# Optimization experiments

Measured on AMD Instinct MI355X. Metric: run time of the kernel, lower is better.

The kernel has to match this reference:

```python
import jax, jax.numpy as jnp
import numpy as np

H = 4                      # num_heads hard-coded in SDHGNN
NAMES = ["self", "cross", "self", "cross"]
POOL_SIZES = [2, 2, 2, 2]
MIN_NGHS = 128             # minium_nghs
EPS = 1e-3                 # InstanceNorm1d eps


def _pw(x, W, b):
    # pointwise Conv1d(kernel=1): [B, Cin, N] -> [B, Cout, N]
    return jnp.einsum('oi,bin->bon', W, x) + b[None, :, None]


def _instnorm(x):
    # InstanceNorm1d (no affine): normalize over N per (B, C)
    m = jnp.mean(x, axis=2, keepdims=True)
    v = jnp.mean((x - m) ** 2, axis=2, keepdims=True)
    return (x - m) * jax.lax.rsqrt(v + EPS)


def _attn_prop(x, src, p):
    # SharedAttentionalPropagation (sharing_attention=False):
    # MultiHeadedAttention + concat + MLP residual update.
    Wq, bq, Wk, bk, Wv, bv, Wm, bm, W1, b1, W2, b2 = p
    B, D, N = x.shape
    dh = D // H
    q = _pw(x, Wq, bq).reshape(B, dh, H, N)
    k = _pw(src, Wk, bk).reshape(B, dh, H, -1)
    v = _pw(src, Wv, bv).reshape(B, dh, H, -1)
    scores = jnp.einsum('bdhn,bdhm->bhnm', q, k) * (dh ** -0.5)
    prob = jax.nn.softmax(scores, axis=-1)                     # [B,H,N,M]
    msg = jnp.einsum('bhnm,bdhm->bdhn', prob, v).reshape(B, D, N)
    msg = _pw(msg, Wm, bm)
    y = jnp.concatenate([x, msg], axis=1)                      # [B,2D,N]
    h = jax.nn.relu(_instnorm(_pw(y, W1, b1)))
    return x + _pw(h, W2, b2), prob


def _gather(x, idx):
    # x: [B,D,N], idx: [B,K] -> [B,D,K]
    return jnp.take_along_axis(
        x, jnp.broadcast_to(idx[:, None, :], (x.shape[0], x.shape[1], idx.shape[1])), axis=2)


def _pool(prob, idx, pool_size):
    # pooling_by_prob (4-D prob branch): mean over heads, sum over queries,
    # top-k by importance, sorted indices, gather global indexes.
    K = idx.shape[1]
    p = prob.mean(axis=1).sum(axis=1)                          # [B,K]
    k = min(max(K // pool_size, MIN_NGHS), K)
    _, top = jax.lax.top_k(p, k)
    top = jnp.sort(top, axis=1)
    return jnp.take_along_axis(idx, top, axis=1)


def setup_inputs() -> dict:
    key = jax.random.key(0)
    B, D, N, L = 2, 128, 2048, 4
    ks = jax.random.split(key, 16)
    s = lambda fan: 1.0 / np.sqrt(fan)
    inp = {
        'x0': jax.random.normal(ks[0], (B, D, N), jnp.float32),
        'x1': jax.random.normal(ks[1], (B, D, N), jnp.float32),
        'Wq': jax.random.normal(ks[2], (L, D, D), jnp.float32) * s(D),
        'bq': jax.random.normal(ks[3], (L, D), jnp.float32) * 0.01,
        'Wk': jax.random.normal(ks[4], (L, D, D), jnp.float32) * s(D),
        'bk': jax.random.normal(ks[5], (L, D), jnp.float32) * 0.01,
        'Wv': jax.random.normal(ks[6], (L, D, D), jnp.float32) * s(D),
        'bv': jax.random.normal(ks[7], (L, D), jnp.float32) * 0.01,
        'Wm': jax.random.normal(ks[8], (L, D, D), jnp.float32) * s(D),
        'bm': jax.random.normal(ks[9], (L, D), jnp.float32) * 0.01,
        'W1': jax.random.normal(ks[10], (L, 2 * D, 2 * D), jnp.float32) * s(2 * D),
        'b1': jax.random.normal(ks[11], (L, 2 * D), jnp.float32) * 0.01,
        'W2': jax.random.normal(ks[12], (L, D, 2 * D), jnp.float32) * s(2 * D),
        'b2': jnp.zeros((L, D), jnp.float32),  # nn.init.constant_(mlp[-1].bias, 0)
    }
    return inp


def reference(x0, x1, Wq, bq, Wk, bk, Wv, bv, Wm, bm, W1, b1, W2, b2):
    B, D, N = x0.shape
    idx0 = jnp.broadcast_to(jnp.arange(N, dtype=jnp.int32)[None], (B, N))
    idx1 = idx0
    for l, (name, ps) in enumerate(zip(NAMES, POOL_SIZES)):
        p = (Wq[l], bq[l], Wk[l], bk[l], Wv[l], bv[l],
             Wm[l], bm[l], W1[l], b1[l], W2[l], b2[l])
        if name == 'self':
            s0, s1 = _gather(x0, idx0), _gather(x1, idx1)
        else:
            s0, s1 = _gather(x1, idx1), _gather(x0, idx0)
        x0, prob0 = _attn_prop(x0, s0, p)
        x1, prob1 = _attn_prop(x1, s1, p)
        if name == 'self':
            idx0 = _pool(prob0, idx0, ps)
            idx1 = _pool(prob1, idx1, ps)
        else:
            idx1 = _pool(prob0, idx1, ps)
            idx0 = _pool(prob1, idx0, ps)
    return jnp.stack([x0, x1], axis=0)   # [2, B, D, N]
```

## Files before the change

kernel.cpp:

```cpp
#include <hip/hip_runtime.h>
#include <cstdint>
#include <cstddef>


#define NB 2
#define ND 128
#define NH 4
#define NN 2048
#define ND2 256
#define DN (ND*NN)
#define BDN (NB*DN)
#define QK_SCALE 0.2550348623f
#define IN_EPS 1e-3f

typedef unsigned short u16;
typedef __attribute__((ext_vector_type(8))) short short8;
typedef __attribute__((ext_vector_type(4))) float f32x4;

__device__ __forceinline__ u16 f2bf(float f) {
    unsigned u = __float_as_uint(f);
    return (u16)((u + 0x7fffu + ((u >> 16) & 1u)) >> 16);
}
__device__ __forceinline__ float bf2f(u16 h) {
    return __uint_as_float(((unsigned)h) << 16);
}
__device__ __forceinline__ float fexp2(float x) {
#if __has_builtin(__builtin_amdgcn_exp2f)
    return __builtin_amdgcn_exp2f(x);
#else
    return exp2f(x);
#endif
}
__device__ __forceinline__ unsigned cvtpk_bf16(float a, float b) {
    unsigned r;
    asm("v_cvt_pk_bf16_f32 %0, %1, %2" : "=v"(r) : "v"(a), "v"(b));
    return r;
}

__global__ __launch_bounds__(256) void init_kernel(
    const float* __restrict__ x0in, const float* __restrict__ x1in,
    float* __restrict__ out, int* __restrict__ idx0, int* __restrict__ idx1)
{
    int tid = blockIdx.x * 256 + threadIdx.x;
    const float4* a = (const float4*)x0in;
    const float4* b = (const float4*)x1in;
    float4* o = (float4*)out;
    o[tid] = a[tid];
    o[BDN/4 + tid] = b[tid];
    if (tid < NB*NN) {
        int v = tid & (NN-1);
        idx0[tid] = v;
        idx1[tid] = v;
    }
}

__global__ __launch_bounds__(256) void wrepack2_kernel(
    const float* __restrict__ Wq, const float* __restrict__ Wk,
    const float* __restrict__ Wv, const float* __restrict__ Wm,
    const float* __restrict__ W1, const float* __restrict__ W2,
    const float* __restrict__ bq, const float* __restrict__ bk,
    const float* __restrict__ bv,
    u16* __restrict__ whi, u16* __restrict__ wlo,
    float* __restrict__ bqp, float* __restrict__ bkp, float* __restrict__ bvp)
{
    int e = blockIdx.x * 256 + threadIdx.x;
    if (e < 655360) {
        int l = e / 163840, r = e - l*163840;
        float v;
        if (r < 49152) {
            int m = r >> 14;
            int rr = r & 16383;
            int o = rr >> 7, c = rr & 127;
            int so = (o & 31)*4 + (o >> 5);
            const float* W = (m == 0) ? Wq : ((m == 1) ? Wk : Wv);
            v = W[l*16384 + so*128 + c];
        } else if (r < 65536) {
            int rr = r - 49152;
            int o = rr >> 7, c = rr & 127;
            int sc = (c & 31)*4 + (c >> 5);
            v = Wm[l*16384 + o*128 + sc];
        } else if (r < 131072) v = W1[l*65536 + r - 65536];
        else                   v = W2[l*32768 + r - 131072];
        u16 hb = f2bf(v);
        whi[e] = hb;
        wlo[e] = f2bf(v - bf2f(hb));
    } else if (e < 656896) {
        int eb = e - 655360;
        int l = eb / 384, rr = eb % 384;
        int which = rr >> 7, o = rr & 127;
        int so = (o & 31)*4 + (o >> 5);
        float v = (which == 0 ? bq : (which == 1 ? bk : bv))[l*128 + so];
        (which == 0 ? bqp : (which == 1 ? bkp : bvp))[l*128 + o] = v;
    }
}

__global__ __launch_bounds__(256) void repack_xh_kernel(
    const float* __restrict__ in, u16* __restrict__ ohi, u16* __restrict__ olo)
{
    __shared__ float tile[32][68];
    int z = blockIdx.y >> 2, cg = blockIdx.y & 3;
    int n0 = blockIdx.x * 64;
    int t = threadIdx.x;
    {
        int i = t >> 3, nc = (t & 7) * 8;
        const float* src = &in[((size_t)z*128 + cg*32 + i)*NN + n0 + nc];
        float4 a = *(const float4*)src;
        float4 b = *(const float4*)(src + 4);
        tile[i][nc+0]=a.x; tile[i][nc+1]=a.y; tile[i][nc+2]=a.z; tile[i][nc+3]=a.w;
        tile[i][nc+4]=b.x; tile[i][nc+5]=b.y; tile[i][nc+6]=b.z; tile[i][nc+7]=b.w;
    }
    __syncthreads();
    int n = t >> 2, c8 = (t & 3) * 8;
    short8 hi, lo;
    #pragma unroll
    for (int j = 0; j < 8; ++j) {
        float v = tile[c8 + j][n];
        u16 h = f2bf(v);
        hi[j] = (short)h;
        lo[j] = (short)f2bf(v - bf2f(h));
    }
    size_t ob = ((size_t)z*NN + n0 + n)*128 + cg*32 + c8;
    *(short8*)&ohi[ob] = hi;
    *(short8*)&olo[ob] = lo;
}

__device__ __forceinline__ void gcore(
    u16* As0, u16* As1, u16* Bs0, u16* Bs1,
    const u16* __restrict__ Whi, const u16* __restrict__ Wlo, int o0, int Cin,
    const u16* __restrict__ B1hi, const u16* __restrict__ B1lo, int s1,
    const u16* __restrict__ B2hi, const u16* __restrict__ B2lo, int s2, int split,
    size_t brow, int n0, const int* __restrict__ idxp, int t, f32x4 acc[2][2])
{
    const int lane = t & 63, w = t >> 6;
    const int l15 = lane & 15, quad = lane >> 4;
    const int wr = (w & 1)*32, wc = (w >> 1)*32;
    const int ao = t >> 2, ak = (t & 3)*8;
    int grow = n0 + ao;
    if (idxp) grow = idxp[grow];

    short8 rA0, rA1, rB0, rB1;
    {
        size_t wa = (size_t)(o0 + ao)*Cin + ak;
        rA0 = *(const short8*)&Whi[wa];
        rA1 = *(const short8*)&Wlo[wa];
        int c = ak;
        const u16 *ph, *pl; size_t off;
        if (c < split) { ph = B1hi; pl = B1lo; off = (brow + grow)*s1 + c; }
        else { ph = B2hi; pl = B2lo; off = (brow + grow)*s2 + (c - split); }
        rB0 = *(const short8*)&ph[off];
        rB1 = *(const short8*)&pl[off];
    }
    for (int kc = 0; kc < Cin; kc += 32) {
        __syncthreads();
        *(short8*)&As0[ao*40 + ak] = rA0;
        *(short8*)&As1[ao*40 + ak] = rA1;
        *(short8*)&Bs0[ao*40 + ak] = rB0;
        *(short8*)&Bs1[ao*40 + ak] = rB1;
        if (kc + 32 < Cin) {
            size_t wa = (size_t)(o0 + ao)*Cin + kc + 32 + ak;
            rA0 = *(const short8*)&Whi[wa];
            rA1 = *(const short8*)&Wlo[wa];
            int c = kc + 32 + ak;
            const u16 *ph, *pl; size_t off;
            if (c < split) { ph = B1hi; pl = B1lo; off = (brow + grow)*s1 + c; }
            else { ph = B2hi; pl = B2lo; off = (brow + grow)*s2 + (c - split); }
            rB0 = *(const short8*)&ph[off];
            rB1 = *(const short8*)&pl[off];
        }
        __syncthreads();
        short8 Ah[2], Al[2], Bh[2], Bl[2];
        #pragma unroll
        for (int a = 0; a < 2; ++a) {
            Ah[a] = *(const short8*)&As0[(wr + a*16 + l15)*40 + quad*8];
            Al[a] = *(const short8*)&As1[(wr + a*16 + l15)*40 + quad*8];
        }
        #pragma unroll
        for (int c = 0; c < 2; ++c) {
            Bh[c] = *(const short8*)&Bs0[(wc + c*16 + l15)*40 + quad*8];
            Bl[c] = *(const short8*)&Bs1[(wc + c*16 + l15)*40 + quad*8];
        }
        #pragma unroll
        for (int a = 0; a < 2; ++a)
            #pragma unroll
            for (int c = 0; c < 2; ++c) {
                acc[a][c] = __builtin_amdgcn_mfma_f32_16x16x32_bf16(Ah[a], Bl[c], acc[a][c], 0,0,0);
                acc[a][c] = __builtin_amdgcn_mfma_f32_16x16x32_bf16(Al[a], Bh[c], acc[a][c], 0,0,0);
                acc[a][c] = __builtin_amdgcn_mfma_f32_16x16x32_bf16(Ah[a], Bh[c], acc[a][c], 0,0,0);
            }
    }
    __syncthreads();
}

__global__ __launch_bounds__(256) void qkv_kernel(
    const u16* __restrict__ Whi, const u16* __restrict__ Wlo,
    const float* __restrict__ bqp, const float* __restrict__ bkp,
    const float* __restrict__ bvp,
    const u16* __restrict__ xphi, const u16* __restrict__ xplo,
    const int* __restrict__ idx0, const int* __restrict__ idx1,
    int cross, int M,
    u16* __restrict__ qthi, u16* __restrict__ qtlo,
    u16* __restrict__ kthi, u16* __restrict__ ktlo,
    u16* __restrict__ vthi, float* __restrict__ p)
{
    __shared__ u16 gsm[10240];
    u16* As0 = gsm;  u16* As1 = gsm + 2560;
    u16* Bs0 = gsm + 5120; u16* Bs1 = gsm + 7680;
    float* tb = (float*)gsm;

    const int z = blockIdx.z;
    const int bx = blockIdx.x;
    const int t = threadIdx.x;
    const int lane = t & 63, w = t >> 6;
    const int l15 = lane & 15, quad = lane >> 4;
    const int wr = (w & 1)*32, wc = (w >> 1)*32;

    int role, o0, n0, nCols;
    const u16 *Wbh, *Wbl;
    const float* bias;
    if (bx < 64) {
        role = 0; o0 = (bx & 1)*64; n0 = (bx >> 1)*64; nCols = NN;
        Wbh = Whi; Wbl = Wlo; bias = bqp;
        if (t < 32) p[(size_t)z*NN + bx*32 + t] = 0.f;
    } else {
        int e = bx - 64;
        int kt = M >> 6;
        int ct = e % kt, rt = e / kt;
        n0 = ct*64; nCols = M;
        if (rt < 2) { role = 1; o0 = rt*64; Wbh = Whi+16384; Wbl = Wlo+16384; bias = bkp; }
        else        { role = 2; o0 = (rt-2)*64; Wbh = Whi+32768; Wbl = Wlo+32768; bias = bvp; }
    }
    size_t brow = (size_t)z * NN;
    const int* idxp = nullptr;
    if (role != 0) {
        int ss = cross ? 1 - (z >> 1) : (z >> 1);
        brow = (size_t)(ss*2 + (z & 1)) * NN;
        idxp = (ss ? idx1 : idx0) + (z & 1)*NN;
    }

    f32x4 acc[2][2];
    #pragma unroll
    for (int a = 0; a < 2; ++a)
        #pragma unroll
        for (int c = 0; c < 2; ++c) acc[a][c] = (f32x4){0.f,0.f,0.f,0.f};

    gcore(As0, As1, Bs0, Bs1, Wbh, Wbl, o0, 128,
          xphi, xplo, 128, xphi, xplo, 128, 128, brow, n0, idxp, t, acc);

    if (role == 2) {
        #pragma unroll
        for (int a = 0; a < 2; ++a)
            #pragma unroll
            for (int c = 0; c < 2; ++c)
                #pragma unroll
                for (int r = 0; r < 4; ++r) {
                    int row = o0 + wr + a*16 + quad*4 + r;
                    int m = n0 + wc + c*16 + l15;
                    float v = acc[a][c][r] + bias[row];
                    vthi[((size_t)(z*4 + (row>>5))*32 + (row&31))*(size_t)M + m] = f2bf(v);
                }
    } else {
        float scale = role ? 1.f : QK_SCALE;
        #pragma unroll
        for (int a = 0; a < 2; ++a)
            #pragma unroll
            for (int c = 0; c < 2; ++c)
                #pragma unroll
                for (int r = 0; r < 4; ++r) {
                    int rl = wr + a*16 + quad*4 + r;
                    tb[rl*66 + wc + c*16 + l15] = acc[a][c][r] + bias[o0 + rl];
                }
        __syncthreads();
        u16* ohi = role ? kthi : qthi;
        u16* olo = role ? ktlo : qtlo;
        int n = t >> 2, rb = (t & 3)*16;
        #pragma unroll
        for (int g = 0; g < 2; ++g) {
            short8 hi, lo;
            #pragma unroll
            for (int j = 0; j < 8; ++j) {
                float v = tb[(rb + g*8 + j)*66 + n] * scale;
                u16 hb = f2bf(v);
                hi[j] = (short)hb;
                lo[j] = (short)f2bf(v - bf2f(hb));
            }
            int rowg = o0 + rb + g*8;
            size_t ob = ((size_t)(z*4 + (rowg >> 5))*nCols + n0 + n)*32 + (rowg & 31);
            *(short8*)&ohi[ob] = hi;
            *(short8*)&olo[ob] = lo;
        }
    }
}

__global__ __launch_bounds__(512, 4) void attn4_kernel(
    const u16* __restrict__ qthi, const u16* __restrict__ qtlo,
    const u16* __restrict__ kthi, const u16* __restrict__ ktlo,
    const u16* __restrict__ vthi, int M,
    u16* __restrict__ msghi, u16* __restrict__ msglo, float* __restrict__ p)
{
    __shared__ u16 kv[14592];
    __shared__ float pcol[2048];
    __shared__ float redm[4][64], redl[4][64];
    __shared__ float rowM[64], rowIV[64];

    u16* ks0 = kv;
    u16* ks1 = kv + 5120;
    u16* vs  = kv + 10240;
    float* obuf = (float*)kv;

    const int t = threadIdx.x;
    const int lane = t & 63, wave = t >> 6;
    const int l15 = lane & 15, quad = lane >> 4;
    const int qp = wave & 1, mh = wave >> 1;
    const int h = blockIdx.y, z = blockIdx.z;
    const int zh = z*4 + h;
    const int n0 = blockIdx.x * 64;

    for (int i = t; i < M; i += 512) pcol[i] = 0.f;

    short8 qBh[2], qBl[2];
    #pragma unroll
    for (int qt = 0; qt < 2; ++qt) {
        size_t qb = ((size_t)zh*NN + n0 + qp*32 + qt*16 + l15)*32 + quad*8;
        qBh[qt] = *(const short8*)&qthi[qb];
        qBl[qt] = *(const short8*)&qtlo[qb];
    }

    const int nch = M >> 7;
    const int sr = t >> 2, sc8 = (t & 3)*8;
    const int vr = t >> 4, vc8 = (t & 15)*8;

    float rm[2] = {-1e30f, -1e30f}, rl[2] = {0.f, 0.f};

    short8 skh, skl, sv;
    {
        size_t gk = ((size_t)zh*M + sr)*32 + sc8;
        skh = *(const short8*)&kthi[gk];
        skl = *(const short8*)&ktlo[gk];
    }

    for (int ch = 0; ch < nch; ++ch) {
        __syncthreads();
        *(short8*)&ks0[sr*40 + sc8] = skh;
        *(short8*)&ks1[sr*40 + sc8] = skl;
        if (ch + 1 < nch) {
            size_t gk = ((size_t)zh*M + ((ch+1) << 7) + sr)*32 + sc8;
            skh = *(const short8*)&kthi[gk];
            skl = *(const short8*)&ktlo[gk];
        }
        __syncthreads();
        #pragma unroll
        for (int qt = 0; qt < 2; ++qt)
            #pragma unroll
            for (int mt = 0; mt < 2; ++mt) {
                int mrow = mh*32 + mt*16 + l15;
                short8 kh = *(const short8*)&ks0[mrow*40 + quad*8];
                short8 kl = *(const short8*)&ks1[mrow*40 + quad*8];
                f32x4 a = {0.f,0.f,0.f,0.f};
                a = __builtin_amdgcn_mfma_f32_16x16x32_bf16(kh, qBl[qt], a, 0,0,0);
                a = __builtin_amdgcn_mfma_f32_16x16x32_bf16(kl, qBh[qt], a, 0,0,0);
                a = __builtin_amdgcn_mfma_f32_16x16x32_bf16(kh, qBh[qt], a, 0,0,0);
                float bm = fmaxf(fmaxf(a[0],a[1]), fmaxf(a[2],a[3]));
                float bs = fexp2(a[0]-bm)+fexp2(a[1]-bm)+fexp2(a[2]-bm)+fexp2(a[3]-bm);
                if (bm > rm[qt]) { rl[qt] = rl[qt]*fexp2(rm[qt]-bm) + bs; rm[qt] = bm; }
                else rl[qt] += bs*fexp2(bm - rm[qt]);
            }
    }

    {
        size_t gk = ((size_t)zh*M + sr)*32 + sc8;
        skh = *(const short8*)&kthi[gk];
        skl = *(const short8*)&ktlo[gk];
        sv  = *(const short8*)&vthi[((size_t)zh*32 + vr)*M + vc8];
    }

    #pragma unroll
    for (int qt = 0; qt < 2; ++qt) {
        #pragma unroll
        for (int off = 16; off <= 32; off <<= 1) {
            float om = __shfl_xor(rm[qt], off);
            float ol = __shfl_xor(rl[qt], off);
            float nm = fmaxf(rm[qt], om);
            rl[qt] = rl[qt]*fexp2(rm[qt]-nm) + ol*fexp2(om-nm);
            rm[qt] = nm;
        }
        if (quad == 0) {
            redm[mh][qp*32 + qt*16 + l15] = rm[qt];
            redl[mh][qp*32 + qt*16 + l15] = rl[qt];
        }
    }
    __syncthreads();
    if (t < 64) {
        float m = redm[0][t], l = redl[0][t];
        #pragma unroll
        for (int w2 = 1; w2 < 4; ++w2) {
            float om = redm[w2][t];
            float nm = fmaxf(m, om);
            l = l*fexp2(m - nm) + redl[w2][t]*fexp2(om - nm);
            m = nm;
        }
        rowM[t] = m;
        rowIV[t] = 1.f / l;
    }
    __syncthreads();
    float myRM[2], myRIV[2];
    #pragma unroll
    for (int qt = 0; qt < 2; ++qt) {
        myRM[qt]  = rowM[qp*32 + qt*16 + l15];
        myRIV[qt] = rowIV[qp*32 + qt*16 + l15];
    }

    f32x4 oa[2][2];
    #pragma unroll
    for (int qt = 0; qt < 2; ++qt)
        #pragma unroll
        for (int dt = 0; dt < 2; ++dt) oa[qt][dt] = (f32x4){0.f,0.f,0.f,0.f};

    const int aA = (l15 + 32*(quad & 1))*4;
    const int aB = aA + 64;
    const bool mtsel = (quad >= 2);

    for (int ch = 0; ch < nch; ++ch) {
        const int m0 = ch << 7;
        __syncthreads();
        *(short8*)&ks0[sr*40 + sc8] = skh;
        *(short8*)&ks1[sr*40 + sc8] = skl;
        *(short8*)&vs[vr*136 + vc8] = sv;
        if (ch + 1 < nch) {
            int m1 = (ch+1) << 7;
            size_t gk = ((size_t)zh*M + m1 + sr)*32 + sc8;
            skh = *(const short8*)&kthi[gk];
            skl = *(const short8*)&ktlo[gk];
            sv  = *(const short8*)&vthi[((size_t)zh*32 + vr)*M + m1 + vc8];
        }
        __syncthreads();

        float pr[2][2][4];
        #pragma unroll
        for (int qt = 0; qt < 2; ++qt)
            #pragma unroll
            for (int mt = 0; mt < 2; ++mt) {
                int mrow = mh*32 + mt*16 + l15;
                short8 kh = *(const short8*)&ks0[mrow*40 + quad*8];
                short8 kl = *(const short8*)&ks1[mrow*40 + quad*8];
                f32x4 a = {0.f,0.f,0.f,0.f};
                a = __builtin_amdgcn_mfma_f32_16x16x32_bf16(kh, qBl[qt], a, 0,0,0);
                a = __builtin_amdgcn_mfma_f32_16x16x32_bf16(kl, qBh[qt], a, 0,0,0);
                a = __builtin_amdgcn_mfma_f32_16x16x32_bf16(kh, qBh[qt], a, 0,0,0);
                #pragma unroll
                for (int r = 0; r < 4; ++r)
                    pr[qt][mt][r] = fexp2(a[r] - myRM[qt]);
            }

        #pragma unroll
        for (int mt = 0; mt < 2; ++mt)
            #pragma unroll
            for (int r = 0; r < 4; ++r) {
                float ps = pr[0][mt][r]*myRIV[0] + pr[1][mt][r]*myRIV[1];
                ps += __shfl_xor(ps, 1);
                ps += __shfl_xor(ps, 2);
                ps += __shfl_xor(ps, 4);
                ps += __shfl_xor(ps, 8);
                if (l15 == 0)
                    atomicAdd(&pcol[m0 + mh*32 + mt*16 + quad*4 + r], ps);
            }

        short8 vA[2];
        #pragma unroll
        for (int dt = 0; dt < 2; ++dt)
            vA[dt] = *(const short8*)&vs[(dt*16 + l15)*136 + mh*32 + quad*8];

        #pragma unroll
        for (int qt = 0; qt < 2; ++qt) {
            unsigned pk00 = cvtpk_bf16(pr[qt][0][0], pr[qt][0][1]);
            unsigned pk01 = cvtpk_bf16(pr[qt][0][2], pr[qt][0][3]);
            unsigned pk10 = cvtpk_bf16(pr[qt][1][0], pr[qt][1][1]);
            unsigned pk11 = cvtpk_bf16(pr[qt][1][2], pr[qt][1][3]);
            unsigned a0 = (unsigned)__builtin_amdgcn_ds_bpermute(aA, (int)pk00);
            unsigned a1 = (unsigned)__builtin_amdgcn_ds_bpermute(aA, (int)pk01);
            unsigned a2 = (unsigned)__builtin_amdgcn_ds_bpermute(aA, (int)pk10);
            unsigned a3 = (unsigned)__builtin_amdgcn_ds_bpermute(aA, (int)pk11);
            unsigned b0 = (unsigned)__builtin_amdgcn_ds_bpermute(aB, (int)pk00);
            unsigned b1 = (unsigned)__builtin_amdgcn_ds_bpermute(aB, (int)pk01);
            unsigned b2 = (unsigned)__builtin_amdgcn_ds_bpermute(aB, (int)pk10);
            unsigned b3 = (unsigned)__builtin_amdgcn_ds_bpermute(aB, (int)pk11);
            union { unsigned u[4]; short8 s; } fb;
            fb.u[0] = mtsel ? a2 : a0;
            fb.u[1] = mtsel ? a3 : a1;
            fb.u[2] = mtsel ? b2 : b0;
            fb.u[3] = mtsel ? b3 : b1;
            #pragma unroll
            for (int dt = 0; dt < 2; ++dt)
                oa[qt][dt] = __builtin_amdgcn_mfma_f32_16x16x32_bf16(vA[dt], fb.s, oa[qt][dt], 0,0,0);
        }
    }
    __syncthreads();

    if (mh > 0) {
        #pragma unroll
        for (int qt = 0; qt < 2; ++qt)
            #pragma unroll
            for (int dt = 0; dt < 2; ++dt)
                #pragma unroll
                for (int r = 0; r < 4; ++r) {
                    int q = qp*32 + qt*16 + l15;
                    int d = dt*16 + quad*4 + r;
                    obuf[((mh-1)*32 + d)*66 + q] = oa[qt][dt][r];
                }
    }
    __syncthreads();
    if (mh == 0) {
        #pragma unroll
        for (int qt = 0; qt < 2; ++qt)
            #pragma unroll
            for (int dt = 0; dt < 2; ++dt)
                #pragma unroll
                for (int r = 0; r < 4; ++r) {
                    int q = qp*32 + qt*16 + l15;
                    int d = dt*16 + quad*4 + r;
                    float v = oa[qt][dt][r];
                    #pragma unroll
                    for (int w2 = 0; w2 < 3; ++w2)
                        v += obuf[(w2*32 + d)*66 + q];
                    obuf[d*66 + q] = v * myRIV[qt];
                }
    }
    __syncthreads();
    {
        int tt = t & 255;
        int n = tt >> 2, i8 = (tt & 3)*8;
        short8 o8;
        if (t < 256) {
            #pragma unroll
            for (int j = 0; j < 8; ++j) o8[j] = (short)f2bf(obuf[(i8+j)*66 + n]);
            *(short8*)&msghi[((size_t)z*NN + n0 + n)*128 + h*32 + i8] = o8;
        } else {
            #pragma unroll
            for (int j = 0; j < 8; ++j) {
                float v = obuf[(i8+j)*66 + n];
                u16 hb = f2bf(v);
                o8[j] = (short)f2bf(v - bf2f(hb));
            }
            *(short8*)&msglo[((size_t)z*NN + n0 + n)*128 + h*32 + i8] = o8;
        }
    }
    for (int i = t; i < M; i += 512)
        atomicAdd(&p[(size_t)z*NN + i], pcol[i]*0.25f);
}

__global__ __launch_bounds__(256) void wm_kernel(
    const u16* __restrict__ Wmh, const u16* __restrict__ Wml,
    const float* __restrict__ bm,
    const u16* __restrict__ msghi, const u16* __restrict__ msglo,
    u16* __restrict__ m2hi, u16* __restrict__ m2lo,
    float* __restrict__ gsum, float* __restrict__ gsq)
{
    __shared__ u16 gsm[10240];
    u16* As0 = gsm;  u16* As1 = gsm + 2560;
    u16* Bs0 = gsm + 5120; u16* Bs1 = gsm + 7680;
    float* tb = (float*)gsm;

    const int z = blockIdx.z, o0 = blockIdx.y*64, n0 = blockIdx.x*64;
    const int t = threadIdx.x;
    const int lane = t & 63, w = t >> 6;
    const int l15 = lane & 15, quad = lane >> 4;
    const int wr = (w & 1)*32, wc = (w >> 1)*32;

    if (blockIdx.x == 0 && blockIdx.y == 0) {
        gsum[z*256 + t] = 0.f;
        gsq[z*256 + t] = 0.f;
    }

    f32x4 acc[2][2];
    #pragma unroll
    for (int a = 0; a < 2; ++a)
        #pragma unroll
        for (int c = 0; c < 2; ++c) acc[a][c] = (f32x4){0.f,0.f,0.f,0.f};
    gcore(As0, As1, Bs0, Bs1, Wmh, Wml, o0, 128,
          msghi, msglo, 128, msghi, msglo, 128, 128,
          (size_t)z*NN, n0, nullptr, t, acc);

    #pragma unroll
    for (int a = 0; a < 2; ++a)
        #pragma unroll
        for (int c = 0; c < 2; ++c)
            #pragma unroll
            for (int r = 0; r < 4; ++r) {
                int rl = wr + a*16 + quad*4 + r;
                tb[rl*66 + wc + c*16 + l15] = acc[a][c][r] + bm[o0 + rl];
            }
    __syncthreads();
    int n = t >> 2, rb = (t & 3)*16;
    #pragma unroll
    for (int g = 0; g < 2; ++g) {
        short8 hi, lo;
        #pragma unroll
        for (int j = 0; j < 8; ++j) {
            float v = tb[(rb + g*8 + j)*66 + n];
            u16 hb = f2bf(v);
            hi[j] = (short)hb;
            lo[j] = (short)f2bf(v - bf2f(hb));
        }
        size_t ob = ((size_t)z*NN + n0 + n)*128 + o0 + rb + g*8;
        *(short8*)&m2hi[ob] = hi;
        *(short8*)&m2lo[ob] = lo;
    }
}

__global__ __launch_bounds__(256) void w1_kernel(
    const u16* __restrict__ W1h, const u16* __restrict__ W1l,
    const float* __restrict__ b1,
    const u16* __restrict__ xphi, const u16* __restrict__ xplo,
    const u16* __restrict__ m2hi, const u16* __restrict__ m2lo,
    float* __restrict__ zf, float* __restrict__ gsum, float* __restrict__ gsq)
{
    __shared__ u16 gsm[10240];
    u16* As0 = gsm;  u16* As1 = gsm + 2560;
    u16* Bs0 = gsm + 5120; u16* Bs1 = gsm + 7680;

    const int z = blockIdx.z, o0 = blockIdx.y*64, n0 = blockIdx.x*64;
    const int t = threadIdx.x;
    const int lane = t & 63, w = t >> 6;
    const int l15 = lane & 15, quad = lane >> 4;
    const int wr = (w & 1)*32, wc = (w >> 1)*32;

    f32x4 acc[2][2];
    #pragma unroll
    for (int a = 0; a < 2; ++a)
        #pragma unroll
        for (int c = 0; c < 2; ++c) acc[a][c] = (f32x4){0.f,0.f,0.f,0.f};
    gcore(As0, As1, Bs0, Bs1, W1h, W1l, o0, 256,
          xphi, xplo, 128, m2hi, m2lo, 128, 128,
          (size_t)z*NN, n0, nullptr, t, acc);

    float ssum[2][4], ssq[2][4];
    #pragma unroll
    for (int a = 0; a < 2; ++a)
        #pragma unroll
        for (int r = 0; r < 4; ++r) { ssum[a][r] = 0.f; ssq[a][r] = 0.f; }
    #pragma unroll
    for (int a = 0; a < 2; ++a)
        #pragma unroll
        for (int c = 0; c < 2; ++c)
            #pragma unroll
            for (int r = 0; r < 4; ++r) {
                int row = o0 + wr + a*16 + quad*4 + r;
                int n = n0 + wc + c*16 + l15;
                float v = acc[a][c][r] + b1[row];
                zf[((size_t)z*256 + row)*NN + n] = v;
                ssum[a][r] += v;
                ssq[a][r] = fmaf(v, v, ssq[a][r]);
            }
    #pragma unroll
    for (int a = 0; a < 2; ++a)
        #pragma unroll
        for (int r = 0; r < 4; ++r) {
            float s = ssum[a][r], q2 = ssq[a][r];
            #pragma unroll
            for (int o = 1; o < 16; o <<= 1) {
                s  += __shfl_xor(s, o);
                q2 += __shfl_xor(q2, o);
            }
            if (l15 == 0) {
                int row = o0 + wr + a*16 + quad*4 + r;
                atomicAdd(&gsum[z*256 + row], s);
                atomicAdd(&gsq[z*256 + row], q2);
            }
        }
}

__global__ __launch_bounds__(256) void hrepack_kernel(
    const float* __restrict__ zf, const float* __restrict__ gsum,
    const float* __restrict__ gsq, u16* __restrict__ hhi, u16* __restrict__ hlo)
{
    __shared__ float tile[32][68];
    int z = blockIdx.y >> 3, cg = blockIdx.y & 7;
    int n0 = blockIdx.x * 64;
    int t = threadIdx.x;
    {
        int i = t >> 3, nc = (t & 7) * 8;
        int c = cg*32 + i;
        float mean = gsum[z*256 + c] * (1.f/NN);
        float var = gsq[z*256 + c] * (1.f/NN) - mean*mean;
        float iv = rsqrtf(var + IN_EPS);
        const float* src = &zf[((size_t)z*256 + c)*NN + n0 + nc];
        float4 a = *(const float4*)src;
        float4 b = *(const float4*)(src + 4);
        float vv[8] = {a.x,a.y,a.z,a.w,b.x,b.y,b.z,b.w};
        #pragma unroll
        for (int j = 0; j < 8; ++j) {
            float v = (vv[j] - mean) * iv;
            tile[i][nc + j] = v > 0.f ? v : 0.f;
        }
    }
    __syncthreads();
    int n = t >> 2, c8 = (t & 3) * 8;
    short8 hi, lo;
    #pragma unroll
    for (int j = 0; j < 8; ++j) {
        float v = tile[c8 + j][n];
        u16 hb = f2bf(v);
        hi[j] = (short)hb;
        lo[j] = (short)f2bf(v - bf2f(hb));
    }
    size_t ob = ((size_t)z*NN + n0 + n)*256 + cg*32 + c8;
    *(short8*)&hhi[ob] = hi;
    *(short8*)&hlo[ob] = lo;
}

__global__ __launch_bounds__(256) void w2_kernel(
    const u16* __restrict__ W2h, const u16* __restrict__ W2l,
    const float* __restrict__ b2,
    const u16* __restrict__ hhi, const u16* __restrict__ hlo,
    float* __restrict__ out, u16* __restrict__ xphi, u16* __restrict__ xplo,
    int writeplanes)
{
    __shared__ u16 gsm[10240];
    u16* As0 = gsm;  u16* As1 = gsm + 2560;
    u16* Bs0 = gsm + 5120; u16* Bs1 = gsm + 7680;
    float* tb = (float*)gsm;

    const int z = blockIdx.z, o0 = blockIdx.y*64, n0 = blockIdx.x*64;
    const int t = threadIdx.x;
    const int lane = t & 63, w = t >> 6;
    const int l15 = lane & 15, quad = lane >> 4;
    const int wr = (w & 1)*32, wc = (w >> 1)*32;

    f32x4 acc[2][2];
    #pragma unroll
    for (int a = 0; a < 2; ++a)
        #pragma unroll
        for (int c = 0; c < 2; ++c) acc[a][c] = (f32x4){0.f,0.f,0.f,0.f};
    gcore(As0, As1, Bs0, Bs1, W2h, W2l, o0, 256,
          hhi, hlo, 256, hhi, hlo, 256, 256,
          (size_t)z*NN, n0, nullptr, t, acc);

    #pragma unroll
    for (int a = 0; a < 2; ++a)
        #pragma unroll
        for (int c = 0; c < 2; ++c)
            #pragma unroll
            for (int r = 0; r < 4; ++r) {
                int rl = wr + a*16 + quad*4 + r;
                int rowg = o0 + rl;
                int n = n0 + wc + c*16 + l15;
                size_t oi = ((size_t)z*128 + rowg)*NN + n;
                float v = acc[a][c][r] + b2[rowg] + out[oi];
                out[oi] = v;
                tb[rl*66 + wc + c*16 + l15] = v;
            }
    __syncthreads();
    if (writeplanes) {
        int n = t >> 2, rb = (t & 3)*16;
        #pragma unroll
        for (int g = 0; g < 2; ++g) {
            short8 hi, lo;
            #pragma unroll
            for (int j = 0; j < 8; ++j) {
                float v = tb[(rb + g*8 + j)*66 + n];
                u16 hb = f2bf(v);
                hi[j] = (short)hb;
                lo[j] = (short)f2bf(v - bf2f(hb));
            }
            size_t ob = ((size_t)z*NN + n0 + n)*128 + o0 + rb + g*8;
            *(short8*)&xphi[ob] = hi;
            *(short8*)&xplo[ob] = lo;
        }
    }
}

__global__ __launch_bounds__(256) void rank_kernel(
    const float* __restrict__ p, int* __restrict__ rank, int M)
{
    int zz = blockIdx.y;
    __shared__ float pv[2048];
    for (int i = threadIdx.x; i < M; i += 256) pv[i] = p[(size_t)zz*NN + i];
    __syncthreads();
    int i = blockIdx.x * 256 + threadIdx.x;
    if (i < M) {
        float pi = pv[i];
        int r = 0;
        for (int j = 0; j < M; ++j) {
            float pj = pv[j];
            r += (pj > pi) ? 1 : ((pj == pi && j < i) ? 1 : 0);
        }
        rank[zz*NN + i] = r;
    }
}

__global__ __launch_bounds__(256) void select_kernel(
    const int* __restrict__ rank, int* __restrict__ idx0, int* __restrict__ idx1,
    int M, int k, int cross)
{
    int z = blockIdx.x;
    int st = z >> 1, b = z & 1;
    int ts = cross ? 1 - st : st;
    int* idx = (ts ? idx1 : idx0) + b * NN;
    const int* rk = rank + z * NN;
    __shared__ int sel[2048], idv[2048], sa[2048], sb[2048];
    int t = threadIdx.x;
    for (int i = t; i < M; i += 256) {
        int s = rk[i] < k ? 1 : 0;
        sel[i] = s;
        sa[i] = s;
        idv[i] = idx[i];
    }
    __syncthreads();
    int* src = sa; int* dst = sb;
    for (int off = 1; off < M; off <<= 1) {
        for (int i = t; i < M; i += 256)
            dst[i] = src[i] + (i >= off ? src[i - off] : 0);
        __syncthreads();
        int* tmp = src; src = dst; dst = tmp;
    }
    for (int i = t; i < M; i += 256)
        if (sel[i]) idx[src[i] - 1] = idv[i];
}

extern "C" void kernel_launch(void* const* d_in, const int* in_sizes, int n_in,
                              void* d_out, int out_size, void* d_ws, size_t ws_size,
                              hipStream_t stream)
{
    const float* x0in = (const float*)d_in[0];
    const float* x1in = (const float*)d_in[1];
    const float* Wq = (const float*)d_in[2];
    const float* bq = (const float*)d_in[3];
    const float* Wk = (const float*)d_in[4];
    const float* bk = (const float*)d_in[5];
    const float* Wv = (const float*)d_in[6];
    const float* bv = (const float*)d_in[7];
    const float* Wm = (const float*)d_in[8];
    const float* bm = (const float*)d_in[9];
    const float* W1 = (const float*)d_in[10];
    const float* b1 = (const float*)d_in[11];
    const float* W2 = (const float*)d_in[12];
    const float* b2 = (const float*)d_in[13];

    float* out = (float*)d_out;
    float* ws  = (float*)d_ws;

    const size_t U = 1048576;
    u16* ub   = (u16*)ws;
    u16* xphi = ub;            u16* xplo = ub + U;
    u16* qthi = ub + 2*U;      u16* qtlo = ub + 3*U;
    u16* kthi = ub + 4*U;      u16* ktlo = ub + 5*U;
    u16* vthi = ub + 6*U;
    u16* msghi = ub + 7*U;     u16* msglo = ub + 8*U;
    u16* m2hi = ub + 9*U;      u16* m2lo = ub + 10*U;
    u16* hhi  = ub + 11*U;     u16* hlo = ub + 13*U;
    u16* whi  = ub + 15*U;     u16* wlo = whi + 655360;
    float* zf = (float*)(ub + 2*U);
    float* ft = (float*)(wlo + 655360);
    float* bqp = ft;           float* bkp = ft + 512;      float* bvp = ft + 1024;
    float* gsum = ft + 1536;   float* gsq = ft + 2560;
    float* p = ft + 3584;
    int* idx0 = (int*)(p + 4*NN);
    int* idx1 = idx0 + NB*NN;
    int* rankb = idx1 + NB*NN;

    init_kernel<<<BDN/4/256, 256, 0, stream>>>(x0in, x1in, out, idx0, idx1);
    wrepack2_kernel<<<2566, 256, 0, stream>>>(Wq, Wk, Wv, Wm, W1, W2, bq, bk, bv,
                                              whi, wlo, bqp, bkp, bvp);
    repack_xh_kernel<<<dim3(32, 16), 256, 0, stream>>>(out, xphi, xplo);

    const int Ms[4] = {2048, 1024, 512, 256};
    for (int l = 0; l < 4; ++l) {
        int M = Ms[l];
        int k_new = (M/2 < 128) ? 128 : M/2;
        int cross = l & 1;
        size_t lw = (size_t)l * 163840;
        const u16* Wlh = whi + lw;  const u16* Wll = wlo + lw;

        qkv_kernel<<<dim3(64 + 4*(M/64), 1, 4), 256, 0, stream>>>(
            Wlh, Wll, bqp + l*128, bkp + l*128, bvp + l*128,
            xphi, xplo, idx0, idx1, cross, M,
            qthi, qtlo, kthi, ktlo, vthi, p);

        attn4_kernel<<<dim3(32, NH, 4), 512, 0, stream>>>(
            qthi, qtlo, kthi, ktlo, vthi, M, msghi, msglo, p);

        wm_kernel<<<dim3(32, 2, 4), 256, 0, stream>>>(
            Wlh + 49152, Wll + 49152, bm + l*128,
            msghi, msglo, m2hi, m2lo, gsum, gsq);

        w1_kernel<<<dim3(32, 4, 4), 256, 0, stream>>>(
            Wlh + 65536, Wll + 65536, b1 + l*256,
            xphi, xplo, m2hi, m2lo, zf, gsum, gsq);

        hrepack_kernel<<<dim3(32, 32), 256, 0, stream>>>(zf, gsum, gsq, hhi, hlo);

        w2_kernel<<<dim3(32, 2, 4), 256, 0, stream>>>(
            Wlh + 131072, Wll + 131072, b2 + l*128,
            hhi, hlo, out, xphi, xplo, (l < 3) ? 1 : 0);

        rank_kernel<<<dim3((M+255)/256, 4), 256, 0, stream>>>(p, rankb, M);
        select_kernel<<<4, 256, 0, stream>>>(rankb, idx0, idx1, M, k_new, cross);
    }
}
```

Before: 542.3 us.

## Load K/V fragments directly from global memory in attention kernel, drop LDS staging

The attention kernel no longer stages K and V chunks through shared memory with register prefetch and two barriers per chunk. Each wave instead loads its own MFMA operand fragments straight from global memory (relying on L1/L2 for reuse across waves), and the MFMA groups are wrapped in s_setprio to favor matrix issue. This removes the per-chunk __syncthreads and LDS traffic, at the cost of redundant global loads across waves, less latency hiding without explicit prefetch, and a dedicated obuf array. The final barrier before the obuf write was also removed, which is safe only because obuf no longer aliases the K/V staging buffer.

```diff
diff --git a/kernel.cpp b/kernel.cpp
--- a/kernel.cpp
+++ b/kernel.cpp
@@ -297,15 +297,10 @@
     const u16* __restrict__ vthi, int M,
     u16* __restrict__ msghi, u16* __restrict__ msglo, float* __restrict__ p)
 {
-    __shared__ u16 kv[14592];
     __shared__ float pcol[2048];
+    __shared__ float obuf[96*66];
     __shared__ float redm[4][64], redl[4][64];
     __shared__ float rowM[64], rowIV[64];
-
-    u16* ks0 = kv;
-    u16* ks1 = kv + 5120;
-    u16* vs  = kv + 10240;
-    float* obuf = (float*)kv;
 
     const int t = threadIdx.x;
     const int lane = t & 63, wave = t >> 6;
@@ -326,51 +321,39 @@
     }
 
     const int nch = M >> 7;
-    const int sr = t >> 2, sc8 = (t & 3)*8;
-    const int vr = t >> 4, vc8 = (t & 15)*8;
+    const size_t kb0 = ((size_t)zh*M + mh*32 + l15)*32 + quad*8;
+    const u16* kbh = kthi + kb0;
+    const u16* kbl = ktlo + kb0;
+    const u16* vb = vthi + ((size_t)zh*32 + l15)*M + mh*32 + quad*8;
 
     float rm[2] = {-1e30f, -1e30f}, rl[2] = {0.f, 0.f};
 
-    short8 skh, skl, sv;
-    {
-        size_t gk = ((size_t)zh*M + sr)*32 + sc8;
-        skh = *(const short8*)&kthi[gk];
-        skl = *(const short8*)&ktlo[gk];
-    }
-
     for (int ch = 0; ch < nch; ++ch) {
-        __syncthreads();
-        *(short8*)&ks0[sr*40 + sc8] = skh;
-        *(short8*)&ks1[sr*40 + sc8] = skl;
-        if (ch + 1 < nch) {
-            size_t gk = ((size_t)zh*M + ((ch+1) << 7) + sr)*32 + sc8;
-            skh = *(const short8*)&kthi[gk];
-            skl = *(const short8*)&ktlo[gk];
-        }
-        __syncthreads();
-        #pragma unroll
-        for (int qt = 0; qt < 2; ++qt)
-            #pragma unroll
-            for (int mt = 0; mt < 2; ++mt) {
-                int mrow = mh*32 + mt*16 + l15;
-                short8 kh = *(const short8*)&ks0[mrow*40 + quad*8];
-                short8 kl = *(const short8*)&ks1[mrow*40 + quad*8];
+        const int co = ch*128*32;
+        #pragma unroll
+        for (int mt = 0; mt < 2; ++mt) {
+            short8 kh = *(const short8*)&kbh[co + mt*512];
+            short8 kl = *(const short8*)&kbl[co + mt*512];
+            __builtin_amdgcn_s_setprio(1);
+            f32x4 av[2];
+            #pragma unroll
+            for (int qt = 0; qt < 2; ++qt) {
                 f32x4 a = {0.f,0.f,0.f,0.f};
                 a = __builtin_amdgcn_mfma_f32_16x16x32_bf16(kh, qBl[qt], a, 0,0,0);
                 a = __builtin_amdgcn_mfma_f32_16x16x32_bf16(kl, qBh[qt], a, 0,0,0);
                 a = __builtin_amdgcn_mfma_f32_16x16x32_bf16(kh, qBh[qt], a, 0,0,0);
+                av[qt] = a;
+            }
+            __builtin_amdgcn_s_setprio(0);
+            #pragma unroll
+            for (int qt = 0; qt < 2; ++qt) {
+                f32x4 a = av[qt];
                 float bm = fmaxf(fmaxf(a[0],a[1]), fmaxf(a[2],a[3]));
                 float bs = fexp2(a[0]-bm)+fexp2(a[1]-bm)+fexp2(a[2]-bm)+fexp2(a[3]-bm);
                 if (bm > rm[qt]) { rl[qt] = rl[qt]*fexp2(rm[qt]-bm) + bs; rm[qt] = bm; }
                 else rl[qt] += bs*fexp2(bm - rm[qt]);
             }
-    }
-
-    {
-        size_t gk = ((size_t)zh*M + sr)*32 + sc8;
-        skh = *(const short8*)&kthi[gk];
-        skl = *(const short8*)&ktlo[gk];
-        sv  = *(const short8*)&vthi[((size_t)zh*32 + vr)*M + vc8];
+        }
     }
 
     #pragma unroll
@@ -421,35 +404,30 @@
 
     for (int ch = 0; ch < nch; ++ch) {
         const int m0 = ch << 7;
-        __syncthreads();
-        *(short8*)&ks0[sr*40 + sc8] = skh;
-        *(short8*)&ks1[sr*40 + sc8] = skl;
-        *(short8*)&vs[vr*136 + vc8] = sv;
-        if (ch + 1 < nch) {
-            int m1 = (ch+1) << 7;
-            size_t gk = ((size_t)zh*M + m1 + sr)*32 + sc8;
-            skh = *(const short8*)&kthi[gk];
-            skl = *(const short8*)&ktlo[gk];
-            sv  = *(const short8*)&vthi[((size_t)zh*32 + vr)*M + m1 + vc8];
-        }
-        __syncthreads();
+        const int co = ch*128*32;
 
         float pr[2][2][4];
         #pragma unroll
-        for (int qt = 0; qt < 2; ++qt)
-            #pragma unroll
-            for (int mt = 0; mt < 2; ++mt) {
-                int mrow = mh*32 + mt*16 + l15;
-                short8 kh = *(const short8*)&ks0[mrow*40 + quad*8];
-                short8 kl = *(const short8*)&ks1[mrow*40 + quad*8];
+        for (int mt = 0; mt < 2; ++mt) {
+            short8 kh = *(const short8*)&kbh[co + mt*512];
+            short8 kl = *(const short8*)&kbl[co + mt*512];
+            __builtin_amdgcn_s_setprio(1);
+            f32x4 av[2];
+            #pragma unroll
+            for (int qt = 0; qt < 2; ++qt) {
                 f32x4 a = {0.f,0.f,0.f,0.f};
                 a = __builtin_amdgcn_mfma_f32_16x16x32_bf16(kh, qBl[qt], a, 0,0,0);
                 a = __builtin_amdgcn_mfma_f32_16x16x32_bf16(kl, qBh[qt], a, 0,0,0);
                 a = __builtin_amdgcn_mfma_f32_16x16x32_bf16(kh, qBh[qt], a, 0,0,0);
+                av[qt] = a;
+            }
+            __builtin_amdgcn_s_setprio(0);
+            #pragma unroll
+            for (int qt = 0; qt < 2; ++qt)
                 #pragma unroll
                 for (int r = 0; r < 4; ++r)
-                    pr[qt][mt][r] = fexp2(a[r] - myRM[qt]);
-            }
+                    pr[qt][mt][r] = fexp2(av[qt][r] - myRM[qt]);
+        }
 
         #pragma unroll
         for (int mt = 0; mt < 2; ++mt)
@@ -467,7 +445,7 @@
         short8 vA[2];
         #pragma unroll
         for (int dt = 0; dt < 2; ++dt)
-            vA[dt] = *(const short8*)&vs[(dt*16 + l15)*136 + mh*32 + quad*8];
+            vA[dt] = *(const short8*)&vb[(size_t)dt*16*M + m0];
 
         #pragma unroll
         for (int qt = 0; qt < 2; ++qt) {
@@ -488,12 +466,13 @@
             fb.u[1] = mtsel ? a3 : a1;
             fb.u[2] = mtsel ? b2 : b0;
             fb.u[3] = mtsel ? b3 : b1;
+            __builtin_amdgcn_s_setprio(1);
             #pragma unroll
             for (int dt = 0; dt < 2; ++dt)
                 oa[qt][dt] = __builtin_amdgcn_mfma_f32_16x16x32_bf16(vA[dt], fb.s, oa[qt][dt], 0,0,0);
-        }
-    }
-    __syncthreads();
+            __builtin_amdgcn_s_setprio(0);
+        }
+    }
 
     if (mh > 0) {
         #pragma unroll
```

Result: no change. 533.0 us (-1.7%).
